# Performance work log

Measured on AMD Instinct MI355X. Metric: run time of the kernel, lower is better.

The kernel has to match this reference:

```python
import jax, jax.numpy as jnp
import numpy as np

D_MODEL = 1024
NHEAD = 16
HEAD_DIM = D_MODEL // NHEAD
EPS = 1e-5


def layer_norm(x, gamma, beta):
    mu = jnp.mean(x, axis=-1, keepdims=True)
    var = jnp.mean(jnp.square(x - mu), axis=-1, keepdims=True)
    return (x - mu) * jax.lax.rsqrt(var + EPS) * gamma + beta


def setup_inputs() -> dict:
    key = jax.random.key(0)
    ks = jax.random.split(key, 12)
    d = D_MODEL
    s = 1.0 / np.sqrt(d)
    return {
        "x": jax.random.normal(ks[0], (4, 2048, d), dtype=jnp.float32),
        "wq": jax.random.normal(ks[1], (d, d), dtype=jnp.float32) * s,
        "wk": jax.random.normal(ks[2], (d, d), dtype=jnp.float32) * s,
        "wv": jax.random.normal(ks[3], (d, d), dtype=jnp.float32) * s,
        "wo": jax.random.normal(ks[4], (d, d), dtype=jnp.float32) * s,
        "bo": jnp.zeros((d,), dtype=jnp.float32),
        "gx": jnp.ones((d,), dtype=jnp.float32),
        "bx": jnp.zeros((d,), dtype=jnp.float32),
        "gf": jnp.ones((d,), dtype=jnp.float32),
        "bf": jnp.zeros((d,), dtype=jnp.float32),
        "w1": jax.random.normal(ks[5], (d, d), dtype=jnp.float32) * s,
        "b1": jnp.zeros((d,), dtype=jnp.float32),
        "w2": jax.random.normal(ks[6], (d, d), dtype=jnp.float32) * s,
        "b2": jnp.zeros((d,), dtype=jnp.float32),
    }


def reference(x, wq, wk, wv, wo, bo, gx, bx, gf, bf, w1, b1, w2, b2):
    B, S, D = x.shape
    H, Dh = NHEAD, HEAD_DIM
    xs = layer_norm(x, gx, bx)
    q = (xs @ wq).reshape(B, S, H, Dh)
    k = (xs @ wk).reshape(B, S, H, Dh)
    v = (xs @ wv).reshape(B, S, H, Dh)
    scores = jnp.einsum("bqhd,bkhd->bhqk", q, k) / jnp.sqrt(jnp.float32(Dh))
    attn = jax.nn.softmax(scores, axis=-1)  # dropout p=0 -> identity
    o = jnp.einsum("bhqk,bkhd->bqhd", attn, v).reshape(B, S, D)
    attn_out = o @ wo + bo
    xt = x + attn_out
    h = layer_norm(xt, gf, bf)
    ffn = jax.nn.relu(h @ w1 + b1) @ w2 + b2
    return xt + ffn
```

## Files before the change

### kernel.cpp

```cpp
#include <hip/hip_runtime.h>
#include <hip/hip_bf16.h>

typedef __bf16 bf16;
typedef bf16 bf16x8 __attribute__((ext_vector_type(8)));
typedef bf16 bf16x4 __attribute__((ext_vector_type(4)));
typedef float f32x4 __attribute__((ext_vector_type(4)));
typedef float f32x16 __attribute__((ext_vector_type(16)));

#define AS1 __attribute__((address_space(1)))
#define AS3 __attribute__((address_space(3)))

static constexpr int SEQ = 2048;
static constexpr int NH  = 16;
static constexpr int DH  = 64;
static constexpr float SCLQ = 0.125f * 1.44269504088896340736f;

__device__ __forceinline__ void gload16(const void* g, void* l) {
  __builtin_amdgcn_global_load_lds((const AS1 void*)g, (AS3 void*)l, 16, 0, 0);
}

__device__ __forceinline__ unsigned pk2(float a, float b) {
  union { bf16 h[2]; unsigned u; } z;
  z.h[0] = (bf16)a; z.h[1] = (bf16)b;
  return z.u;
}

__device__ __forceinline__ void plswap(unsigned &a, unsigned &b) {
  asm volatile("v_permlane32_swap_b32 %0, %1" : "+v"(a), "+v"(b));
}

#define MFMA32(d, a, b) d = __builtin_amdgcn_mfma_f32_32x32x16_bf16(a, b, d, 0, 0, 0)

__global__ __launch_bounds__(256) void prep_w(
    const float* __restrict__ w0, const float* __restrict__ w1,
    const float* __restrict__ w2, const float* __restrict__ w3,
    const float* __restrict__ w4, const float* __restrict__ w5,
    bf16* __restrict__ dst)
{
  __shared__ float tile[64][65];
  int bid = blockIdx.x;
  int wi = bid >> 8;
  int tl = bid & 255;
  int tk = (tl >> 4) << 6;
  int tn = (tl & 15) << 6;
  const float* W = w0;
  if (wi == 1) W = w1; else if (wi == 2) W = w2; else if (wi == 3) W = w3;
  else if (wi == 4) W = w4; else if (wi == 5) W = w5;
  int t = threadIdx.x;
  #pragma unroll
  for (int rep = 0; rep < 16; ++rep) {
    int idx = rep * 256 + t;
    int i = idx >> 6, j = idx & 63;
    tile[i][j] = W[(size_t)(tk + i) * 1024 + tn + j];
  }
  __syncthreads();
  bf16* out = dst + (size_t)wi * 1024 * 1024;
  #pragma unroll
  for (int rep = 0; rep < 16; ++rep) {
    int idx = rep * 256 + t;
    int i = idx >> 6, j = idx & 63;
    out[(size_t)(tn + i) * 1024 + tk + j] = (bf16)tile[j][i];
  }
}

__global__ __launch_bounds__(256) void ln_k(
    const float* __restrict__ x, const float* __restrict__ g,
    const float* __restrict__ bb, bf16* __restrict__ out)
{
  int row = blockIdx.x;
  int t = threadIdx.x;
  float4 v = ((const float4*)(x + (size_t)row * 1024))[t];
  float s  = v.x + v.y + v.z + v.w;
  float s2 = v.x * v.x + v.y * v.y + v.z * v.z + v.w * v.w;
  #pragma unroll
  for (int m = 1; m < 64; m <<= 1) { s += __shfl_xor(s, m); s2 += __shfl_xor(s2, m); }
  __shared__ float red[8];
  int w = t >> 6;
  if ((t & 63) == 0) { red[w] = s; red[4 + w] = s2; }
  __syncthreads();
  s  = red[0] + red[1] + red[2] + red[3];
  s2 = red[4] + red[5] + red[6] + red[7];
  float mu  = s * (1.0f / 1024.0f);
  float var = s2 * (1.0f / 1024.0f) - mu * mu;
  float rst = rsqrtf(var + 1e-5f);
  float4 gv = ((const float4*)g)[t];
  float4 bv = ((const float4*)bb)[t];
  bf16x4 o;
  o[0] = (bf16)((v.x - mu) * rst * gv.x + bv.x);
  o[1] = (bf16)((v.y - mu) * rst * gv.y + bv.y);
  o[2] = (bf16)((v.z - mu) * rst * gv.z + bv.z);
  o[3] = (bf16)((v.w - mu) * rst * gv.w + bv.w);
  *(bf16x4*)(out + (size_t)row * 1024 + t * 4) = o;
}

template<int EPI, int NT>
__global__ __launch_bounds__(256) void gemm_k(
    const bf16* __restrict__ A, const bf16* __restrict__ Bt,
    const float* __restrict__ bias, const float* __restrict__ res,
    float* __restrict__ outf, bf16* __restrict__ outb)
{
  __shared__ bf16 lA[128 * 64];
  __shared__ bf16 lB[128 * 64];
  int t = threadIdx.x;
  int wg = blockIdx.x;
  int swz = (wg & 7) * (NT * 8) + (wg >> 3);
  int mt = swz / NT, nt = swz % NT;
  int lane = t & 63, w = t >> 6;
  int l16 = lane & 15, lh = lane >> 4;
  int wr = w >> 1, wc = w & 1;

  f32x4 acc[4][4] = {};
  const size_t mbase = (size_t)mt * 128;
  const size_t nbase = (size_t)nt * 128;
  int u = t & 7;

  for (int ks = 0; ks < 16; ++ks) {
    int k0 = ks * 64;
    #pragma unroll
    for (int i = 0; i < 4; ++i) {
      int row = i * 32 + (t >> 3);
      int up = u ^ (row & 7);
      gload16(A  + (mbase + row) * 1024 + k0 + up * 8, lA + i * 2048 + w * 512);
      gload16(Bt + (nbase + row) * 1024 + k0 + up * 8, lB + i * 2048 + w * 512);
    }
    __syncthreads();
    #pragma unroll
    for (int kc = 0; kc < 2; ++kc) {
      bf16x8 af[4], bfr[4];
      #pragma unroll
      for (int mi = 0; mi < 4; ++mi) {
        int row = wr * 64 + mi * 16 + l16;
        af[mi] = *(const bf16x8*)(lA + row * 64 + (((kc * 4 + lh) ^ (row & 7)) * 8));
      }
      #pragma unroll
      for (int ni = 0; ni < 4; ++ni) {
        int row = wc * 64 + ni * 16 + l16;
        bfr[ni] = *(const bf16x8*)(lB + row * 64 + (((kc * 4 + lh) ^ (row & 7)) * 8));
      }
      #pragma unroll
      for (int mi = 0; mi < 4; ++mi)
        #pragma unroll
        for (int ni = 0; ni < 4; ++ni)
          acc[mi][ni] = __builtin_amdgcn_mfma_f32_16x16x32_bf16(af[mi], bfr[ni], acc[mi][ni], 0, 0, 0);
    }
    __syncthreads();
  }

  int mrow0 = mt * 128 + wr * 64;
  int ncol0 = nt * 128 + wc * 64;
  #pragma unroll
  for (int mi = 0; mi < 4; ++mi) {
    #pragma unroll
    for (int ni = 0; ni < 4; ++ni) {
      if constexpr (EPI == 0) {
        int gcol = ncol0 + ni * 16 + l16;
        int which = gcol >> 10;
        int col = gcol & 1023;
        int h = col >> 6, dh = col & 63;
        bf16* dst = outb + (size_t)which * (size_t)(4 * NH * SEQ * DH);
        if (which == 2) {
          int s0 = mrow0 + mi * 16 + lh * 4;
          int b = s0 >> 11, s = s0 & 2047;
          bf16x4 pkv;
          #pragma unroll
          for (int r = 0; r < 4; ++r) pkv[r] = (bf16)acc[mi][ni][r];
          *(bf16x4*)(dst + (((size_t)((b * NH + h) * DH + dh)) << 11) + s) = pkv;
        } else {
          #pragma unroll
          for (int r = 0; r < 4; ++r) {
            int grow = mrow0 + mi * 16 + lh * 4 + r;
            int b = grow >> 11, s = grow & 2047;
            float v = acc[mi][ni][r];
            if (which == 0) v *= SCLQ;
            dst[(((size_t)((b * NH + h) * SEQ + s)) << 6) + dh] = (bf16)v;
          }
        }
      } else {
        #pragma unroll
        for (int r = 0; r < 4; ++r) {
          int grow = mrow0 + mi * 16 + lh * 4 + r;
          int gcol = ncol0 + ni * 16 + l16;
          float v = acc[mi][ni][r];
          if constexpr (EPI == 2) {
            size_t idx = (size_t)grow * 1024 + gcol;
            outf[idx] = v + bias[gcol] + res[idx];
          } else {
            size_t idx = (size_t)grow * 1024 + gcol;
            float z = v + bias[gcol];
            outb[idx] = (bf16)(z > 0.f ? z : 0.f);
          }
        }
      }
    }
  }
}

__global__ __launch_bounds__(256, 2) void attn_k(
    const bf16* __restrict__ q, const bf16* __restrict__ kk,
    const bf16* __restrict__ vt, bf16* __restrict__ o)
{
  __shared__ bf16 lK[2][4096];
  __shared__ bf16 lV[4][4096];

  int t = threadIdx.x;
  int lane = t & 63, w = t >> 6;
  int l31 = lane & 31, hi = lane >> 5;
  int bid = blockIdx.x;
  int swz = (bid & 7) * 64 + (bid >> 3);
  int bh = swz >> 3, qt = swz & 7;
  int q0 = qt * 256 + w * 64;
  size_t bhS = (size_t)bh * SEQ;

  const bf16* qrow0 = q + (bhS + q0 + l31) * 64 + hi * 8;
  const bf16* qrow1 = qrow0 + 32 * 64;
  bf16x8 aq0[4], aq1[4];
  #pragma unroll
  for (int ks = 0; ks < 4; ++ks) {
    aq0[ks] = *(const bf16x8*)(qrow0 + ks * 16);
    aq1[ks] = *(const bf16x8*)(qrow1 + ks * 16);
  }

  int srow = t >> 3;
  int u8 = (t & 7) ^ (srow & 7);
  const bf16* kSrc = kk + (bhS + srow) * 64 + u8 * 8;
  const bf16* vSrc = vt + ((size_t)bh * 64 + srow) * SEQ + u8 * 8;

  f32x16 oa00 = {}, oa01 = {}, oa10 = {}, oa11 = {};
  float lsum0 = 0.f, lsum1 = 0.f;
  unsigned cvA0[4][4], cvA1[4][4], cvB0[4][4], cvB1[4][4];

  gload16(kSrc,            &lK[0][w * 512]);
  gload16(kSrc + 2048,     &lK[0][2048 + w * 512]);
  gload16(vSrc,            &lV[0][w * 512]);
  gload16(vSrc + 32 * SEQ, &lV[0][2048 + w * 512]);
  __syncthreads();

#define ATTN_ITER(T, CVO0, CVO1, CVN0, CVN1, PREF, PV)                        \
  do {                                                                        \
    const int T_ = (T);                                                       \
    const bf16* bK  = &lK[T_ & 1][0];                                         \
    const bf16* bVp = &lV[(T_ - 1) & 3][0];                                   \
    if (PREF) {                                                               \
      bf16* nK = &lK[(T_ + 1) & 1][0];                                        \
      bf16* nV = &lV[(T_ + 1) & 3][0];                                        \
      const bf16* ks2 = kSrc + (size_t)(T_ + 1) * 4096;                       \
      const bf16* vs2 = vSrc + (T_ + 1) * 64;                                 \
      gload16(ks2,            nK + w * 512);                                  \
      gload16(ks2 + 2048,     nK + 2048 + w * 512);                           \
      gload16(vs2,            nV + w * 512);                                  \
      gload16(vs2 + 32 * SEQ, nV + 2048 + w * 512);                           \
    }                                                                         \
    f32x16 sA0 = {}, sB0 = {}, sA1 = {}, sB1 = {};                            \
    __builtin_amdgcn_s_setprio(1);                                            \
    _Pragma("unroll")                                                         \
    for (int ks = 0; ks < 4; ++ks) {                                          \
      int u = ((2 * ks + hi) ^ (l31 & 7)) * 8;                                \
      bf16x8 k0 = *(const bf16x8*)(bK + l31 * 64 + u);                        \
      bf16x8 k1 = *(const bf16x8*)(bK + (32 + l31) * 64 + u);                 \
      MFMA32(sA0, k0, aq0[ks]); MFMA32(sA1, k0, aq1[ks]);                     \
      MFMA32(sB0, k1, aq0[ks]); MFMA32(sB1, k1, aq1[ks]);                     \
    }                                                                         \
    __builtin_amdgcn_s_setprio(0);                                            \
    _Pragma("unroll")                                                         \
    for (int ks = 0; ks < 4; ++ks) {                                          \
      if (PV) {                                                               \
        int u = ((2 * ks + hi) ^ (l31 & 7)) * 8;                              \
        bf16x8 v0 = *(const bf16x8*)(bVp + l31 * 64 + u);                     \
        bf16x8 v1 = *(const bf16x8*)(bVp + (32 + l31) * 64 + u);              \
        union { unsigned u4[4]; bf16x8 v; } a0, a1;                           \
        a0.u4[0] = CVO0[ks][0]; a0.u4[1] = CVO0[ks][1];                       \
        a0.u4[2] = CVO0[ks][2]; a0.u4[3] = CVO0[ks][3];                       \
        a1.u4[0] = CVO1[ks][0]; a1.u4[1] = CVO1[ks][1];                       \
        a1.u4[2] = CVO1[ks][2]; a1.u4[3] = CVO1[ks][3];                       \
        MFMA32(oa00, a0.v, v0); MFMA32(oa01, a0.v, v1);                       \
        MFMA32(oa10, a1.v, v0); MFMA32(oa11, a1.v, v1);                       \
      }                                                                       \
      float e0[8], e1[8];                                                     \
      _Pragma("unroll")                                                       \
      for (int j = 0; j < 8; ++j) {                                           \
        e0[j] = __builtin_amdgcn_exp2f((ks < 2 ? sA0 : sB0)[(ks & 1) * 8 + j]); \
        e1[j] = __builtin_amdgcn_exp2f((ks < 2 ? sA1 : sB1)[(ks & 1) * 8 + j]); \
      }                                                                       \
      lsum0 += ((e0[0] + e0[1]) + (e0[2] + e0[3])) + ((e0[4] + e0[5]) + (e0[6] + e0[7])); \
      lsum1 += ((e1[0] + e1[1]) + (e1[2] + e1[3])) + ((e1[4] + e1[5]) + (e1[6] + e1[7])); \
      unsigned X0 = pk2(e0[0], e0[1]), X1 = pk2(e0[2], e0[3]);                \
      unsigned Y0 = pk2(e0[4], e0[5]), Y1 = pk2(e0[6], e0[7]);                \
      plswap(X0, Y0); plswap(X1, Y1);                                         \
      CVN0[ks][0] = X0; CVN0[ks][1] = X1; CVN0[ks][2] = Y0; CVN0[ks][3] = Y1; \
      unsigned Z0 = pk2(e1[0], e1[1]), Z1 = pk2(e1[2], e1[3]);                \
      unsigned W0 = pk2(e1[4], e1[5]), W1 = pk2(e1[6], e1[7]);                \
      plswap(Z0, W0); plswap(Z1, W1);                                         \
      CVN1[ks][0] = Z0; CVN1[ks][1] = Z1; CVN1[ks][2] = W0; CVN1[ks][3] = W1; \
    }                                                                         \
    __syncthreads();                                                          \
  } while (0)

  ATTN_ITER(0, cvB0, cvB1, cvA0, cvA1, true, false);
  for (int kt = 1; kt < 31; kt += 2) {
    ATTN_ITER(kt,     cvA0, cvA1, cvB0, cvB1, true, true);
    ATTN_ITER(kt + 1, cvB0, cvB1, cvA0, cvA1, true, true);
  }
  ATTN_ITER(31, cvA0, cvA1, cvB0, cvB1, false, true);
#undef ATTN_ITER

  {
    const bf16* bVp = &lV[3][0];
    __builtin_amdgcn_s_setprio(1);
    #pragma unroll
    for (int ks = 0; ks < 4; ++ks) {
      int u = ((2 * ks + hi) ^ (l31 & 7)) * 8;
      bf16x8 v0 = *(const bf16x8*)(bVp + l31 * 64 + u);
      bf16x8 v1 = *(const bf16x8*)(bVp + (32 + l31) * 64 + u);
      union { unsigned u4[4]; bf16x8 v; } a0, a1;
      a0.u4[0] = cvB0[ks][0]; a0.u4[1] = cvB0[ks][1];
      a0.u4[2] = cvB0[ks][2]; a0.u4[3] = cvB0[ks][3];
      a1.u4[0] = cvB1[ks][0]; a1.u4[1] = cvB1[ks][1];
      a1.u4[2] = cvB1[ks][2]; a1.u4[3] = cvB1[ks][3];
      MFMA32(oa00, a0.v, v0); MFMA32(oa01, a0.v, v1);
      MFMA32(oa10, a1.v, v0); MFMA32(oa11, a1.v, v1);
    }
    __builtin_amdgcn_s_setprio(0);
  }

  lsum0 += __shfl_xor(lsum0, 32);
  lsum1 += __shfl_xor(lsum1, 32);
  float inv0 = 1.0f / lsum0;
  float inv1 = 1.0f / lsum1;
  int bb = bh >> 4, hh = bh & 15;
  size_t obase = ((size_t)bb * SEQ + q0) * 1024 + (size_t)hh * 64;
  #pragma unroll
  for (int r = 0; r < 16; ++r) {
    int qrw = (r & 3) + 8 * (r >> 2) + 4 * hi;
    float iv0 = __shfl(inv0, qrw);
    float iv1 = __shfl(inv1, qrw);
    size_t b0 = obase + (size_t)qrw * 1024;
    size_t b1 = obase + (size_t)(32 + qrw) * 1024;
    o[b0 + l31]      = (bf16)(oa00[r] * iv0);
    o[b0 + 32 + l31] = (bf16)(oa01[r] * iv0);
    o[b1 + l31]      = (bf16)(oa10[r] * iv1);
    o[b1 + 32 + l31] = (bf16)(oa11[r] * iv1);
  }
}

extern "C" void kernel_launch(void* const* d_in, const int* in_sizes, int n_in,
                              void* d_out, int out_size, void* d_ws, size_t ws_size,
                              hipStream_t stream) {
  const float* x   = (const float*)d_in[0];
  const float* wq  = (const float*)d_in[1];
  const float* wk  = (const float*)d_in[2];
  const float* wv  = (const float*)d_in[3];
  const float* wo  = (const float*)d_in[4];
  const float* bo  = (const float*)d_in[5];
  const float* gx  = (const float*)d_in[6];
  const float* bx  = (const float*)d_in[7];
  const float* gf  = (const float*)d_in[8];
  const float* bfp = (const float*)d_in[9];
  const float* w1  = (const float*)d_in[10];
  const float* b1  = (const float*)d_in[11];
  const float* w2  = (const float*)d_in[12];
  const float* b2  = (const float*)d_in[13];

  char* ws = (char*)d_ws;
  const size_t MB = 1024 * 1024;
  bf16*  wT  = (bf16*)ws;
  bf16*  xs  = (bf16*)(ws + 12 * MB);
  bf16*  qb  = (bf16*)(ws + 28 * MB);
  bf16*  kb  = (bf16*)(ws + 44 * MB);
  bf16*  vtb = (bf16*)(ws + 60 * MB);
  bf16*  ob  = (bf16*)(ws + 12 * MB);
  float* xt  = (float*)(ws + 28 * MB);
  bf16*  hb  = (bf16*)(ws + 60 * MB);
  bf16*  a1  = (bf16*)(ws + 12 * MB);
  float* out = (float*)d_out;

  prep_w<<<1536, 256, 0, stream>>>(wq, wk, wv, wo, w1, w2, wT);
  ln_k<<<8192, 256, 0, stream>>>(x, gx, bx, xs);
  gemm_k<0, 24><<<1536, 256, 0, stream>>>(xs, wT, nullptr, nullptr, nullptr, qb);
  attn_k<<<512, 256, 0, stream>>>(qb, kb, vtb, ob);
  gemm_k<2, 8><<<512, 256, 0, stream>>>(ob, wT + (size_t)3 * MB, bo, x, xt, nullptr);
  ln_k<<<8192, 256, 0, stream>>>(xt, gf, bfp, hb);
  gemm_k<3, 8><<<512, 256, 0, stream>>>(hb, wT + (size_t)4 * MB, b1, nullptr, nullptr, a1);
  gemm_k<2, 8><<<512, 256, 0, stream>>>(a1, wT + (size_t)5 * MB, b2, xt, out, nullptr);
}
```

Baseline: 270.8 us.

## Triple-buffer K/V tiles with vmcnt-based waits and in-tile PV

Restructures the attention inner loop so each tile computes QK, exp and PV on its own K/V buffer, replacing the old software pipeline that delayed PV by one tile. K and V now share a three-stage buffer with prefetch two tiles ahead. The full __syncthreads is replaced by explicit s_waitcnt vmcnt counts plus s_barrier, so loads for later tiles can stay in flight. This removes the carried register state for delayed P fragments but puts exp and PV on the critical path of each tile, and relies on hand-counted vmcnt values being correct.

```diff
diff --git a/kernel.cpp b/kernel.cpp
--- a/kernel.cpp
+++ b/kernel.cpp
@@ -199,8 +199,8 @@
     const bf16* __restrict__ q, const bf16* __restrict__ kk,
     const bf16* __restrict__ vt, bf16* __restrict__ o)
 {
-  __shared__ bf16 lK[2][4096];
-  __shared__ bf16 lV[4][4096];
+  __shared__ bf16 lK[3][4096];
+  __shared__ bf16 lV[3][4096];
 
   int t = threadIdx.x;
   int lane = t & 63, w = t >> 6;
@@ -225,102 +225,119 @@
   const bf16* kSrc = kk + (bhS + srow) * 64 + u8 * 8;
   const bf16* vSrc = vt + ((size_t)bh * 64 + srow) * SEQ + u8 * 8;
 
+#define STAGE(BUF, T)                                                         \
+  do {                                                                        \
+    const bf16* ks_ = kSrc + (size_t)(T) * 4096;                              \
+    const bf16* vs_ = vSrc + (T) * 64;                                        \
+    gload16(ks_,            &lK[BUF][w * 512]);                               \
+    gload16(ks_ + 2048,     &lK[BUF][2048 + w * 512]);                        \
+    gload16(vs_,            &lV[BUF][w * 512]);                               \
+    gload16(vs_ + 32 * SEQ, &lV[BUF][2048 + w * 512]);                        \
+  } while (0)
+
   f32x16 oa00 = {}, oa01 = {}, oa10 = {}, oa11 = {};
+  const f32x16 FZ = {};
   float lsum0 = 0.f, lsum1 = 0.f;
-  unsigned cvA0[4][4], cvA1[4][4], cvB0[4][4], cvB1[4][4];
-
-  gload16(kSrc,            &lK[0][w * 512]);
-  gload16(kSrc + 2048,     &lK[0][2048 + w * 512]);
-  gload16(vSrc,            &lV[0][w * 512]);
-  gload16(vSrc + 32 * SEQ, &lV[0][2048 + w * 512]);
-  __syncthreads();
-
-#define ATTN_ITER(T, CVO0, CVO1, CVN0, CVN1, PREF, PV)                        \
+
+#define TILE(T, CUR, STG, DOSTG, VMSTR)                                       \
   do {                                                                        \
-    const int T_ = (T);                                                       \
-    const bf16* bK  = &lK[T_ & 1][0];                                         \
-    const bf16* bVp = &lV[(T_ - 1) & 3][0];                                   \
-    if (PREF) {                                                               \
-      bf16* nK = &lK[(T_ + 1) & 1][0];                                        \
-      bf16* nV = &lV[(T_ + 1) & 3][0];                                        \
-      const bf16* ks2 = kSrc + (size_t)(T_ + 1) * 4096;                       \
-      const bf16* vs2 = vSrc + (T_ + 1) * 64;                                 \
-      gload16(ks2,            nK + w * 512);                                  \
-      gload16(ks2 + 2048,     nK + 2048 + w * 512);                           \
-      gload16(vs2,            nV + w * 512);                                  \
-      gload16(vs2 + 32 * SEQ, nV + 2048 + w * 512);                           \
-    }                                                                         \
-    f32x16 sA0 = {}, sB0 = {}, sA1 = {}, sB1 = {};                            \
+    if (DOSTG) STAGE(STG, (T) + 2);                                           \
+    const bf16* bK = &lK[CUR][0];                                             \
+    const bf16* bV = &lV[CUR][0];                                             \
+    f32x16 sA0, sB0, sA1, sB1;                                                \
     __builtin_amdgcn_s_setprio(1);                                            \
     _Pragma("unroll")                                                         \
     for (int ks = 0; ks < 4; ++ks) {                                          \
       int u = ((2 * ks + hi) ^ (l31 & 7)) * 8;                                \
       bf16x8 k0 = *(const bf16x8*)(bK + l31 * 64 + u);                        \
       bf16x8 k1 = *(const bf16x8*)(bK + (32 + l31) * 64 + u);                 \
-      MFMA32(sA0, k0, aq0[ks]); MFMA32(sA1, k0, aq1[ks]);                     \
-      MFMA32(sB0, k1, aq0[ks]); MFMA32(sB1, k1, aq1[ks]);                     \
+      if (ks == 0) {                                                          \
+        sA0 = __builtin_amdgcn_mfma_f32_32x32x16_bf16(k0, aq0[0], FZ, 0, 0, 0); \
+        sA1 = __builtin_amdgcn_mfma_f32_32x32x16_bf16(k0, aq1[0], FZ, 0, 0, 0); \
+        sB0 = __builtin_amdgcn_mfma_f32_32x32x16_bf16(k1, aq0[0], FZ, 0, 0, 0); \
+        sB1 = __builtin_amdgcn_mfma_f32_32x32x16_bf16(k1, aq1[0], FZ, 0, 0, 0); \
+      } else {                                                                \
+        MFMA32(sA0, k0, aq0[ks]); MFMA32(sA1, k0, aq1[ks]);                   \
+        MFMA32(sB0, k1, aq0[ks]); MFMA32(sB1, k1, aq1[ks]);                   \
+      }                                                                       \
     }                                                                         \
     __builtin_amdgcn_s_setprio(0);                                            \
+    unsigned cv0[4][4], cv1[4][4];                                            \
+    {                                                                         \
+      float p[32];                                                            \
+      _Pragma("unroll")                                                       \
+      for (int i = 0; i < 16; ++i) {                                          \
+        p[i]      = __builtin_amdgcn_exp2f(sA0[i]);                           \
+        p[16 + i] = __builtin_amdgcn_exp2f(sB0[i]);                           \
+      }                                                                       \
+      float t8[8];                                                            \
+      _Pragma("unroll")                                                       \
+      for (int i = 0; i < 8; ++i)                                             \
+        t8[i] = (p[4 * i] + p[4 * i + 1]) + (p[4 * i + 2] + p[4 * i + 3]);    \
+      lsum0 += ((t8[0] + t8[1]) + (t8[2] + t8[3])) + ((t8[4] + t8[5]) + (t8[6] + t8[7])); \
+      _Pragma("unroll")                                                       \
+      for (int ks = 0; ks < 4; ++ks) {                                        \
+        int g = 8 * ks;                                                       \
+        unsigned X0 = pk2(p[g],     p[g + 1]), X1 = pk2(p[g + 2], p[g + 3]);  \
+        unsigned Y0 = pk2(p[g + 4], p[g + 5]), Y1 = pk2(p[g + 6], p[g + 7]);  \
+        plswap(X0, Y0); plswap(X1, Y1);                                       \
+        cv0[ks][0] = X0; cv0[ks][1] = X1; cv0[ks][2] = Y0; cv0[ks][3] = Y1;   \
+      }                                                                       \
+    }                                                                         \
+    {                                                                         \
+      float p[32];                                                            \
+      _Pragma("unroll")                                                       \
+      for (int i = 0; i < 16; ++i) {                                          \
+        p[i]      = __builtin_amdgcn_exp2f(sA1[i]);                           \
+        p[16 + i] = __builtin_amdgcn_exp2f(sB1[i]);                           \
+      }                                                                       \
+      float t8[8];                                                            \
+      _Pragma("unroll")                                                       \
+      for (int i = 0; i < 8; ++i)                                             \
+        t8[i] = (p[4 * i] + p[4 * i + 1]) + (p[4 * i + 2] + p[4 * i + 3]);    \
+      lsum1 += ((t8[0] + t8[1]) + (t8[2] + t8[3])) + ((t8[4] + t8[5]) + (t8[6] + t8[7])); \
+      _Pragma("unroll")                                                       \
+      for (int ks = 0; ks < 4; ++ks) {                                        \
+        int g = 8 * ks;                                                       \
+        unsigned X0 = pk2(p[g],     p[g + 1]), X1 = pk2(p[g + 2], p[g + 3]);  \
+        unsigned Y0 = pk2(p[g + 4], p[g + 5]), Y1 = pk2(p[g + 6], p[g + 7]);  \
+        plswap(X0, Y0); plswap(X1, Y1);                                       \
+        cv1[ks][0] = X0; cv1[ks][1] = X1; cv1[ks][2] = Y0; cv1[ks][3] = Y1;   \
+      }                                                                       \
+    }                                                                         \
+    __builtin_amdgcn_s_setprio(1);                                            \
     _Pragma("unroll")                                                         \
     for (int ks = 0; ks < 4; ++ks) {                                          \
-      if (PV) {                                                               \
-        int u = ((2 * ks + hi) ^ (l31 & 7)) * 8;                              \
-        bf16x8 v0 = *(const bf16x8*)(bVp + l31 * 64 + u);                     \
-        bf16x8 v1 = *(const bf16x8*)(bVp + (32 + l31) * 64 + u);              \
-        union { unsigned u4[4]; bf16x8 v; } a0, a1;                           \
-        a0.u4[0] = CVO0[ks][0]; a0.u4[1] = CVO0[ks][1];                       \
-        a0.u4[2] = CVO0[ks][2]; a0.u4[3] = CVO0[ks][3];                       \
-        a1.u4[0] = CVO1[ks][0]; a1.u4[1] = CVO1[ks][1];                       \
-        a1.u4[2] = CVO1[ks][2]; a1.u4[3] = CVO1[ks][3];                       \
-        MFMA32(oa00, a0.v, v0); MFMA32(oa01, a0.v, v1);                       \
-        MFMA32(oa10, a1.v, v0); MFMA32(oa11, a1.v, v1);                       \
-      }                                                                       \
-      float e0[8], e1[8];                                                     \
-      _Pragma("unroll")                                                       \
-      for (int j = 0; j < 8; ++j) {                                           \
-        e0[j] = __builtin_amdgcn_exp2f((ks < 2 ? sA0 : sB0)[(ks & 1) * 8 + j]); \
-        e1[j] = __builtin_amdgcn_exp2f((ks < 2 ? sA1 : sB1)[(ks & 1) * 8 + j]); \
-      }                                                                       \
-      lsum0 += ((e0[0] + e0[1]) + (e0[2] + e0[3])) + ((e0[4] + e0[5]) + (e0[6] + e0[7])); \
-      lsum1 += ((e1[0] + e1[1]) + (e1[2] + e1[3])) + ((e1[4] + e1[5]) + (e1[6] + e1[7])); \
-      unsigned X0 = pk2(e0[0], e0[1]), X1 = pk2(e0[2], e0[3]);                \
-      unsigned Y0 = pk2(e0[4], e0[5]), Y1 = pk2(e0[6], e0[7]);                \
-      plswap(X0, Y0); plswap(X1, Y1);                                         \
-      CVN0[ks][0] = X0; CVN0[ks][1] = X1; CVN0[ks][2] = Y0; CVN0[ks][3] = Y1; \
-      unsigned Z0 = pk2(e1[0], e1[1]), Z1 = pk2(e1[2], e1[3]);                \
-      unsigned W0 = pk2(e1[4], e1[5]), W1 = pk2(e1[6], e1[7]);                \
-      plswap(Z0, W0); plswap(Z1, W1);                                         \
-      CVN1[ks][0] = Z0; CVN1[ks][1] = Z1; CVN1[ks][2] = W0; CVN1[ks][3] = W1; \
+      int u = ((2 * ks + hi) ^ (l31 & 7)) * 8;                                \
+      bf16x8 v0 = *(const bf16x8*)(bV + l31 * 64 + u);                        \
+      bf16x8 v1 = *(const bf16x8*)(bV + (32 + l31) * 64 + u);                 \
+      union { unsigned u4[4]; bf16x8 v; } a0, a1;                             \
+      a0.u4[0] = cv0[ks][0]; a0.u4[1] = cv0[ks][1];                           \
+      a0.u4[2] = cv0[ks][2]; a0.u4[3] = cv0[ks][3];                           \
+      a1.u4[0] = cv1[ks][0]; a1.u4[1] = cv1[ks][1];                           \
+      a1.u4[2] = cv1[ks][2]; a1.u4[3] = cv1[ks][3];                           \
+      MFMA32(oa00, a0.v, v0); MFMA32(oa01, a0.v, v1);                         \
+      MFMA32(oa10, a1.v, v0); MFMA32(oa11, a1.v, v1);                         \
     }                                                                         \
-    __syncthreads();                                                          \
+    __builtin_amdgcn_s_setprio(0);                                            \
+    asm volatile(VMSTR ::: "memory");                                         \
+    __builtin_amdgcn_s_barrier();                                             \
   } while (0)
 
-  ATTN_ITER(0, cvB0, cvB1, cvA0, cvA1, true, false);
-  for (int kt = 1; kt < 31; kt += 2) {
-    ATTN_ITER(kt,     cvA0, cvA1, cvB0, cvB1, true, true);
-    ATTN_ITER(kt + 1, cvB0, cvB1, cvA0, cvA1, true, true);
-  }
-  ATTN_ITER(31, cvA0, cvA1, cvB0, cvB1, false, true);
-#undef ATTN_ITER
-
-  {
-    const bf16* bVp = &lV[3][0];
-    __builtin_amdgcn_s_setprio(1);
-    #pragma unroll
-    for (int ks = 0; ks < 4; ++ks) {
-      int u = ((2 * ks + hi) ^ (l31 & 7)) * 8;
-      bf16x8 v0 = *(const bf16x8*)(bVp + l31 * 64 + u);
-      bf16x8 v1 = *(const bf16x8*)(bVp + (32 + l31) * 64 + u);
-      union { unsigned u4[4]; bf16x8 v; } a0, a1;
-      a0.u4[0] = cvB0[ks][0]; a0.u4[1] = cvB0[ks][1];
-      a0.u4[2] = cvB0[ks][2]; a0.u4[3] = cvB0[ks][3];
-      a1.u4[0] = cvB1[ks][0]; a1.u4[1] = cvB1[ks][1];
-      a1.u4[2] = cvB1[ks][2]; a1.u4[3] = cvB1[ks][3];
-      MFMA32(oa00, a0.v, v0); MFMA32(oa01, a0.v, v1);
-      MFMA32(oa10, a1.v, v0); MFMA32(oa11, a1.v, v1);
-    }
-    __builtin_amdgcn_s_setprio(0);
-  }
+  STAGE(0, 0);
+  STAGE(1, 1);
+  asm volatile("s_waitcnt vmcnt(4)" ::: "memory");
+  __builtin_amdgcn_s_barrier();
+
+  for (int kt = 0; kt < 30; kt += 3) {
+    TILE(kt,     0, 2, true, "s_waitcnt vmcnt(4)");
+    TILE(kt + 1, 1, 0, true, "s_waitcnt vmcnt(4)");
+    TILE(kt + 2, 2, 1, true, "s_waitcnt vmcnt(4)");
+  }
+  TILE(30, 0, 0, false, "s_waitcnt vmcnt(0)");
+  TILE(31, 1, 0, false, "s_nop 0");
+#undef TILE
+#undef STAGE
 
   lsum0 += __shfl_xor(lsum0, 32);
   lsum1 += __shfl_xor(lsum1, 32);
```

New measurement: 283.8 us. +4.8%, slower.
